# Optimization experiments

Hardware: AMD Instinct MI355X
Metric: run time of the kernel (lower is better)

## Reference

```python
import jax, jax.numpy as jnp
import numpy as np

N_NODES = 50000
N_EDGES = 1600000
N_GRAPHS = 512
NEG_SLOPE = 0.2


def _glorot(key, shape):
    fan_in, fan_out = shape[0], shape[-1]
    lim = jnp.sqrt(6.0 / (fan_in + fan_out))
    return jax.random.uniform(key, shape, jnp.float32, -lim, lim)


def setup_inputs() -> dict:
    key = jax.random.key(0)
    ks = jax.random.split(key, 12)
    x = jax.random.normal(ks[0], (N_NODES, 5), jnp.float32)
    edge_index = jax.random.randint(ks[1], (2, N_EDGES), 0, N_NODES, jnp.int64)
    batch = jnp.sort(jax.random.randint(ks[2], (N_NODES,), 0, N_GRAPHS, jnp.int64))
    # layer0: in=5 -> heads=4, out=16 (concat -> 64)
    W1l = _glorot(ks[3], (5, 64))
    W1r = _glorot(ks[4], (5, 64))
    att1 = _glorot(ks[5], (4, 16))
    b1 = jnp.zeros((64,), jnp.float32)
    # layer1: in=64 -> heads=1, out=64 (no concat)
    W2l = _glorot(ks[6], (64, 64))
    W2r = _glorot(ks[7], (64, 64))
    att2 = _glorot(ks[8], (1, 64))
    b2 = jnp.zeros((64,), jnp.float32)
    # predictor Linear(64, 1)
    Wp = _glorot(ks[9], (64, 1))
    bp = jnp.zeros((1,), jnp.float32)
    return {"x": x, "edge_index": edge_index, "batch": batch,
            "W1l": W1l, "W1r": W1r, "att1": att1, "b1": b1,
            "W2l": W2l, "W2r": W2r, "att2": att2, "b2": b2,
            "Wp": Wp, "bp": bp}


def _gatv2(x, src, dst, Wl, Wr, att, b, heads, dim, concat):
    n = x.shape[0]
    xl = (x @ Wl).reshape(n, heads, dim)  # source transform
    xr = (x @ Wr).reshape(n, heads, dim)  # target transform
    s = jax.nn.leaky_relu(xl[src] + xr[dst], NEG_SLOPE)      # [E,H,D]
    e = jnp.einsum('ehd,hd->eh', s, att)                      # [E,H]
    m = jax.ops.segment_max(e, dst, num_segments=n)           # segment softmax
    p = jnp.exp(e - m[dst])
    denom = jax.ops.segment_sum(p, dst, num_segments=n) + 1e-16
    alpha = p / denom[dst]                                    # [E,H]
    out = jax.ops.segment_sum(xl[src] * alpha[..., None], dst, num_segments=n)
    out = out.reshape(n, heads * dim) if concat else out.mean(axis=1)
    return out + b


def reference(x, edge_index, batch, W1l, W1r, att1, b1, W2l, W2r, att2, b2, Wp, bp):
    n = x.shape[0]
    # PyG GATv2Conv default add_self_loops=True
    loop = jnp.arange(n, dtype=edge_index.dtype)
    src = jnp.concatenate([edge_index[0], loop])
    dst = jnp.concatenate([edge_index[1], loop])
    h = _gatv2(x, src, dst, W1l, W1r, att1, b1, heads=4, dim=16, concat=True)
    h = jax.nn.relu(h)  # dropout is identity at eval
    h = _gatv2(h, src, dst, W2l, W2r, att2, b2, heads=1, dim=64, concat=False)
    h = jax.nn.relu(h)
    # global_mean_pool over graph ids
    sums = jax.ops.segment_sum(h, batch, num_segments=N_GRAPHS)
    cnt = jax.ops.segment_sum(jnp.ones((n,), h.dtype), batch, num_segments=N_GRAPHS)
    pooled = sums / jnp.maximum(cnt, 1.0)[:, None]
    return (pooled @ Wp + bp).squeeze(-1)
```

## Files before the change

kernel.cpp:

```cpp
#include <hip/hip_runtime.h>
#include <hip/hip_fp16.h>
#include <math.h>

#define NEG_SLOPE 0.2f
#define BUCKET 96

__device__ __forceinline__ float lrelu(float x) { return fmaxf(x, NEG_SLOPE * x); }

template <int CTRL>
__device__ __forceinline__ float dpp_add(float x) {
    int t = __builtin_amdgcn_update_dpp(0, __float_as_int(x), CTRL, 0xF, 0xF, false);
    return x + __int_as_float(t);
}

__device__ __forceinline__ float red8(float x) {
    x = dpp_add<0xB1>(x);
    x = dpp_add<0x4E>(x);
    x = dpp_add<0x141>(x);
    return x;
}

__device__ __forceinline__ float red32(float x) {
    x = red8(x);
    x = dpp_add<0x140>(x);
    x += __shfl_xor(x, 16, 64);
    return x;
}

__global__ void k_scatter(const int* __restrict__ ei, int* __restrict__ cnt,
                          int* __restrict__ ssrc, int E, int ET, int n, int nsub) {
    int part = blockIdx.x & 7;
    int sub  = blockIdx.x >> 3;
    int lo = (int)(((long long)part * n) >> 3);
    int hi = (int)(((long long)(part + 1) * n) >> 3);
    int stride = nsub * blockDim.x;
    for (int e = sub * blockDim.x + threadIdx.x; e < ET; e += stride) {
        int dst = (e < E) ? ei[E + e] : (e - E);
        if (dst >= lo && dst < hi) {
            int src = (e < E) ? ei[e] : dst;
            int pos = atomicAdd(&cnt[dst], 1);
            if (pos < BUCKET) ssrc[dst * BUCKET + pos] = src;
        }
    }
}

__global__ void k_t1(const float* __restrict__ x,
                     const float* __restrict__ W1l, const float* __restrict__ W1r,
                     __half* __restrict__ xl, float* __restrict__ xr, int n) {
    __shared__ float sWl[5 * 64], sWr[5 * 64];
    int t = threadIdx.x;
    for (int i = t; i < 5 * 64; i += blockDim.x) { sWl[i] = W1l[i]; sWr[i] = W1r[i]; }
    __syncthreads();
    int tid = blockIdx.x * blockDim.x + t;
    if (tid >= n * 64) return;
    int node = tid >> 6, j = tid & 63;
    const float* xp = x + node * 5;
    float x0 = xp[0], x1 = xp[1], x2 = xp[2], x3 = xp[3], x4 = xp[4];
    float al = x0 * sWl[j] + x1 * sWl[64 + j] + x2 * sWl[128 + j] + x3 * sWl[192 + j] + x4 * sWl[256 + j];
    float ar = x0 * sWr[j] + x1 * sWr[64 + j] + x2 * sWr[128 + j] + x3 * sWr[192 + j] + x4 * sWr[256 + j];
    xl[tid] = __float2half(al);
    xr[tid] = ar;
}

__global__ void __launch_bounds__(256, 8)
k_gat1(const int* __restrict__ ssrc, const int* __restrict__ deg,
       const __half* __restrict__ xl, const float* __restrict__ xr,
       const float* __restrict__ att1, const float* __restrict__ b1,
       const float* __restrict__ W2l, const float* __restrict__ W2r,
       __half* __restrict__ hl, float* __restrict__ hr, int n) {
    __shared__ float sh[4][64];
    int t = threadIdx.x;
    int wid = t >> 6, lane = t & 63;
    int node = __builtin_amdgcn_readfirstlane(blockIdx.x * 4 + wid);
    int half = lane >> 5, l31 = lane & 31;
    if (node < n) {
        float2 xrd  = *(const float2*)(xr + (size_t)node * 64 + 2 * l31);
        float2 attv = *(const float2*)(att1 + 2 * l31);
        float m = -INFINITY, den = 0.f, acc0 = 0.f, acc1 = 0.f;
        const int* bp_ = ssrc + (size_t)node * BUCKET;
        int end = deg[node]; if (end > BUCKET) end = BUCKET;
        int k = 0;
        for (; k + 15 < end; k += 16) {
            float2 a[8];
#pragma unroll
            for (int j = 0; j < 8; ++j) {
                int s0 = bp_[k + 2 * j], s1 = bp_[k + 2 * j + 1];
                int sj = half ? s1 : s0;
                a[j] = __half22float2(*(const __half2*)(xl + ((unsigned)sj << 6) + 2u * l31));
            }
            float s[8];
#pragma unroll
            for (int j = 0; j < 8; ++j)
                s[j] = lrelu(a[j].x + xrd.x) * attv.x + lrelu(a[j].y + xrd.y) * attv.y;
#pragma unroll
            for (int j = 0; j < 8; ++j) s[j] = red8(s[j]);
            float mb = fmaxf(fmaxf(fmaxf(s[0], s[1]), fmaxf(s[2], s[3])),
                             fmaxf(fmaxf(s[4], s[5]), fmaxf(s[6], s[7])));
            float mn = fmaxf(m, mb);
            float sc = __expf(m - mn);
            den *= sc; acc0 *= sc; acc1 *= sc;
#pragma unroll
            for (int j = 0; j < 8; ++j) {
                float p = __expf(s[j] - mn);
                den += p; acc0 += p * a[j].x; acc1 += p * a[j].y;
            }
            m = mn;
        }
        for (; k + 7 < end; k += 8) {
            float2 a[4];
#pragma unroll
            for (int j = 0; j < 4; ++j) {
                int s0 = bp_[k + 2 * j], s1 = bp_[k + 2 * j + 1];
                int sj = half ? s1 : s0;
                a[j] = __half22float2(*(const __half2*)(xl + ((unsigned)sj << 6) + 2u * l31));
            }
            float s[4];
#pragma unroll
            for (int j = 0; j < 4; ++j)
                s[j] = lrelu(a[j].x + xrd.x) * attv.x + lrelu(a[j].y + xrd.y) * attv.y;
#pragma unroll
            for (int j = 0; j < 4; ++j) s[j] = red8(s[j]);
            float mb = fmaxf(fmaxf(s[0], s[1]), fmaxf(s[2], s[3]));
            float mn = fmaxf(m, mb);
            float sc = __expf(m - mn);
            den *= sc; acc0 *= sc; acc1 *= sc;
#pragma unroll
            for (int j = 0; j < 4; ++j) {
                float p = __expf(s[j] - mn);
                den += p; acc0 += p * a[j].x; acc1 += p * a[j].y;
            }
            m = mn;
        }
        for (; k + 1 < end; k += 2) {
            int s0 = bp_[k], s1 = bp_[k + 1];
            int sj = half ? s1 : s0;
            float2 a = __half22float2(*(const __half2*)(xl + ((unsigned)sj << 6) + 2u * l31));
            float s = lrelu(a.x + xrd.x) * attv.x + lrelu(a.y + xrd.y) * attv.y;
            s = red8(s);
            float mn = fmaxf(m, s);
            float sc = __expf(m - mn);
            float p  = __expf(s - mn);
            den = den * sc + p;
            acc0 = acc0 * sc + p * a.x;
            acc1 = acc1 * sc + p * a.y;
            m = mn;
        }
        if (k < end) {
            int sj = bp_[k];
            float2 a = __half22float2(*(const __half2*)(xl + ((unsigned)sj << 6) + 2u * l31));
            float s = lrelu(a.x + xrd.x) * attv.x + lrelu(a.y + xrd.y) * attv.y;
            s = red8(s);
            if (half == 0) {
                float mn = fmaxf(m, s);
                float sc = __expf(m - mn);
                float p  = __expf(s - mn);
                den = den * sc + p;
                acc0 = acc0 * sc + p * a.x;
                acc1 = acc1 * sc + p * a.y;
                m = mn;
            }
        }
        float m_o  = __shfl_xor(m, 32, 64);
        float d_o  = __shfl_xor(den, 32, 64);
        float a0_o = __shfl_xor(acc0, 32, 64);
        float a1_o = __shfl_xor(acc1, 32, 64);
        float mf = fmaxf(m, m_o);
        float sc = __expf(m - mf), sco = __expf(m_o - mf);
        float denf = den * sc + d_o * sco + 1e-16f;
        float2 b = *(const float2*)(b1 + 2 * l31);
        float o0 = fmaxf((acc0 * sc + a0_o * sco) / denf + b.x, 0.f);
        float o1 = fmaxf((acc1 * sc + a1_o * sco) / denf + b.y, 0.f);
        if (half == 0) *(float2*)&sh[wid][2 * l31] = make_float2(o0, o1);
    }
    __syncthreads();
    if (node >= n) return;
    float accl = 0.f, accr = 0.f;
#pragma unroll 8
    for (int q = 0; q < 64; ++q) {
        float hv = sh[wid][q];
        accl += hv * W2l[q * 64 + lane];
        accr += hv * W2r[q * 64 + lane];
    }
    hl[(size_t)node * 64 + lane] = __float2half(accl);
    hr[(size_t)node * 64 + lane] = accr;
}

__global__ void __launch_bounds__(256, 8)
k_gat2(const int* __restrict__ ssrc, const int* __restrict__ deg,
       const __half* __restrict__ hl, const float* __restrict__ hr,
       const float* __restrict__ att2, const float* __restrict__ b2,
       const int* __restrict__ batch,
       float* __restrict__ pooled, float* __restrict__ cnt, int n) {
    int node = __builtin_amdgcn_readfirstlane((blockIdx.x * blockDim.x + threadIdx.x) >> 6);
    if (node >= n) return;
    int lane = threadIdx.x & 63;
    int half = lane >> 5, l31 = lane & 31;
    float2 hrd  = *(const float2*)(hr + (size_t)node * 64 + 2 * l31);
    float2 attv = *(const float2*)(att2 + 2 * l31);
    float m = -INFINITY, den = 0.f, acc0 = 0.f, acc1 = 0.f;
    const int* bp_ = ssrc + (size_t)node * BUCKET;
    int end = deg[node]; if (end > BUCKET) end = BUCKET;
    int k = 0;
    for (; k + 15 < end; k += 16) {
        float2 a[8];
#pragma unroll
        for (int j = 0; j < 8; ++j) {
            int s0 = bp_[k + 2 * j], s1 = bp_[k + 2 * j + 1];
            int sj = half ? s1 : s0;
            a[j] = __half22float2(*(const __half2*)(hl + ((unsigned)sj << 6) + 2u * l31));
        }
        float s[8];
#pragma unroll
        for (int j = 0; j < 8; ++j)
            s[j] = lrelu(a[j].x + hrd.x) * attv.x + lrelu(a[j].y + hrd.y) * attv.y;
#pragma unroll
        for (int j = 0; j < 8; ++j) s[j] = red32(s[j]);
        float mb = fmaxf(fmaxf(fmaxf(s[0], s[1]), fmaxf(s[2], s[3])),
                         fmaxf(fmaxf(s[4], s[5]), fmaxf(s[6], s[7])));
        float mn = fmaxf(m, mb);
        float sc = __expf(m - mn);
        den *= sc; acc0 *= sc; acc1 *= sc;
#pragma unroll
        for (int j = 0; j < 8; ++j) {
            float p = __expf(s[j] - mn);
            den += p; acc0 += p * a[j].x; acc1 += p * a[j].y;
        }
        m = mn;
    }
    for (; k + 7 < end; k += 8) {
        float2 a[4];
#pragma unroll
        for (int j = 0; j < 4; ++j) {
            int s0 = bp_[k + 2 * j], s1 = bp_[k + 2 * j + 1];
            int sj = half ? s1 : s0;
            a[j] = __half22float2(*(const __half2*)(hl + ((unsigned)sj << 6) + 2u * l31));
        }
        float s[4];
#pragma unroll
        for (int j = 0; j < 4; ++j)
            s[j] = lrelu(a[j].x + hrd.x) * attv.x + lrelu(a[j].y + hrd.y) * attv.y;
#pragma unroll
        for (int j = 0; j < 4; ++j) s[j] = red32(s[j]);
        float mb = fmaxf(fmaxf(s[0], s[1]), fmaxf(s[2], s[3]));
        float mn = fmaxf(m, mb);
        float sc = __expf(m - mn);
        den *= sc; acc0 *= sc; acc1 *= sc;
#pragma unroll
        for (int j = 0; j < 4; ++j) {
            float p = __expf(s[j] - mn);
            den += p; acc0 += p * a[j].x; acc1 += p * a[j].y;
        }
        m = mn;
    }
    for (; k + 1 < end; k += 2) {
        int s0 = bp_[k], s1 = bp_[k + 1];
        int sj = half ? s1 : s0;
        float2 a = __half22float2(*(const __half2*)(hl + ((unsigned)sj << 6) + 2u * l31));
        float s = lrelu(a.x + hrd.x) * attv.x + lrelu(a.y + hrd.y) * attv.y;
        s = red32(s);
        float mn = fmaxf(m, s);
        float sc = __expf(m - mn);
        float p  = __expf(s - mn);
        den = den * sc + p;
        acc0 = acc0 * sc + p * a.x;
        acc1 = acc1 * sc + p * a.y;
        m = mn;
    }
    if (k < end) {
        int sj = bp_[k];
        float2 a = __half22float2(*(const __half2*)(hl + ((unsigned)sj << 6) + 2u * l31));
        float s = lrelu(a.x + hrd.x) * attv.x + lrelu(a.y + hrd.y) * attv.y;
        s = red32(s);
        if (half == 0) {
            float mn = fmaxf(m, s);
            float sc = __expf(m - mn);
            float p  = __expf(s - mn);
            den = den * sc + p;
            acc0 = acc0 * sc + p * a.x;
            acc1 = acc1 * sc + p * a.y;
            m = mn;
        }
    }
    float m_o  = __shfl_xor(m, 32, 64);
    float d_o  = __shfl_xor(den, 32, 64);
    float a0_o = __shfl_xor(acc0, 32, 64);
    float a1_o = __shfl_xor(acc1, 32, 64);
    float mf = fmaxf(m, m_o);
    float sc = __expf(m - mf), sco = __expf(m_o - mf);
    float denf = den * sc + d_o * sco + 1e-16f;
    float2 b = *(const float2*)(b2 + 2 * l31);
    float o0 = fmaxf((acc0 * sc + a0_o * sco) / denf + b.x, 0.f);
    float o1 = fmaxf((acc1 * sc + a1_o * sco) / denf + b.y, 0.f);
    int g = batch[node];
    atomicAdd(&pooled[(size_t)g * 64 + 2 * l31 + half], half ? o1 : o0);
    if (lane == 0) atomicAdd(&cnt[g], 1.0f);
}

__global__ void k_predict(const float* __restrict__ pooled, const float* __restrict__ cnt,
                          const float* __restrict__ Wp, const float* __restrict__ bp,
                          float* __restrict__ out, int G) {
    int tid = blockIdx.x * blockDim.x + threadIdx.x;
    int g = tid >> 6;
    if (g >= G) return;
    int lane = threadIdx.x & 63;
    float c = cnt[g];
    if (c < 1.f) c = 1.f;
    float v = (pooled[(size_t)g * 64 + lane] / c) * Wp[lane];
#pragma unroll
    for (int off = 32; off > 0; off >>= 1) v += __shfl_down(v, off, 64);
    if (lane == 0) out[g] = v + bp[0];
}

extern "C" void kernel_launch(void* const* d_in, const int* in_sizes, int n_in,
                              void* d_out, int out_size, void* d_ws, size_t ws_size,
                              hipStream_t stream) {
    const float* x    = (const float*)d_in[0];
    const int*   ei   = (const int*)d_in[1];
    const int*   batch= (const int*)d_in[2];
    const float* W1l  = (const float*)d_in[3];
    const float* W1r  = (const float*)d_in[4];
    const float* att1 = (const float*)d_in[5];
    const float* b1   = (const float*)d_in[6];
    const float* W2l  = (const float*)d_in[7];
    const float* W2r  = (const float*)d_in[8];
    const float* att2 = (const float*)d_in[9];
    const float* b2   = (const float*)d_in[10];
    const float* Wp   = (const float*)d_in[11];
    const float* bp   = (const float*)d_in[12];
    float* out = (float*)d_out;

    const int n  = in_sizes[0] / 5;
    const int E  = in_sizes[1] / 2;
    const int ET = E + n;
    const int G  = out_size;

    char* ws = (char*)d_ws;
    size_t off = 0;
    auto alloc_b = [&](size_t bytes) { void* p = (void*)(ws + off); off += (bytes + 15) & ~15ull; return p; };
    __half* xl    = (__half*)alloc_b((size_t)n * 64 * 2);
    float*  xr    = (float*)alloc_b((size_t)n * 64 * 4);
    __half* hl    = (__half*)alloc_b((size_t)n * 64 * 2);
    float*  hr    = (float*)alloc_b((size_t)n * 64 * 4);
    float*  pooled= (float*)alloc_b((size_t)G * 64 * 4);
    float*  cntf  = (float*)alloc_b((size_t)G * 4);
    int*    deg   = (int*)alloc_b((size_t)n * 4);
    int*    ssrc  = (int*)alloc_b((size_t)n * BUCKET * 4);

    size_t zero_bytes = (size_t)((char*)deg - (char*)pooled) + (size_t)n * 4;
    (void)hipMemsetAsync(pooled, 0, zero_bytes, stream);

    const int B = 256;
    const int NSUB = 256;

    k_scatter<<<8 * NSUB, B, 0, stream>>>(ei, deg, ssrc, E, ET, n, NSUB);

    k_t1<<<(n * 64 + B - 1) / B, B, 0, stream>>>(x, W1l, W1r, xl, xr, n);

    k_gat1<<<(n + 3) / 4, B, 0, stream>>>(ssrc, deg, xl, xr, att1, b1, W2l, W2r, hl, hr, n);
    k_gat2<<<((size_t)n * 64 + B - 1) / B, B, 0, stream>>>(ssrc, deg, hl, hr, att2, b2, batch, pooled, cntf, n);
    k_predict<<<(G * 64 + B - 1) / B, B, 0, stream>>>(pooled, cntf, Wp, bp, out, G);
}
```

Baseline: 358.4 us.

## Process 8 edges per wave with 8 lanes each using 16-byte gathers

After: 382.7 us. 1.07x slower.

```diff
diff --git a/kernel.cpp b/kernel.cpp
--- a/kernel.cpp
+++ b/kernel.cpp
@@ -17,13 +17,6 @@
     x = dpp_add<0xB1>(x);
     x = dpp_add<0x4E>(x);
     x = dpp_add<0x141>(x);
-    return x;
-}
-
-__device__ __forceinline__ float red32(float x) {
-    x = red8(x);
-    x = dpp_add<0x140>(x);
-    x += __shfl_xor(x, 16, 64);
     return x;
 }
 
@@ -62,7 +55,7 @@
     xr[tid] = ar;
 }
 
-__global__ void __launch_bounds__(256, 8)
+__global__ void __launch_bounds__(256, 5)
 k_gat1(const int* __restrict__ ssrc, const int* __restrict__ deg,
        const __half* __restrict__ xl, const float* __restrict__ xr,
        const float* __restrict__ att1, const float* __restrict__ b1,
@@ -72,105 +65,100 @@
     int t = threadIdx.x;
     int wid = t >> 6, lane = t & 63;
     int node = __builtin_amdgcn_readfirstlane(blockIdx.x * 4 + wid);
-    int half = lane >> 5, l31 = lane & 31;
+    int g = lane >> 3, c = lane & 7;
     if (node < n) {
-        float2 xrd  = *(const float2*)(xr + (size_t)node * 64 + 2 * l31);
-        float2 attv = *(const float2*)(att1 + 2 * l31);
-        float m = -INFINITY, den = 0.f, acc0 = 0.f, acc1 = 0.f;
+        float xrd[8], attv[8];
+        {
+            float4 v0 = *(const float4*)(xr + (size_t)node * 64 + 8 * c);
+            float4 v1 = *(const float4*)(xr + (size_t)node * 64 + 8 * c + 4);
+            xrd[0] = v0.x; xrd[1] = v0.y; xrd[2] = v0.z; xrd[3] = v0.w;
+            xrd[4] = v1.x; xrd[5] = v1.y; xrd[6] = v1.z; xrd[7] = v1.w;
+            float4 a0 = *(const float4*)(att1 + 8 * c);
+            float4 a1 = *(const float4*)(att1 + 8 * c + 4);
+            attv[0] = a0.x; attv[1] = a0.y; attv[2] = a0.z; attv[3] = a0.w;
+            attv[4] = a1.x; attv[5] = a1.y; attv[6] = a1.z; attv[7] = a1.w;
+        }
+        float m = -1e30f, den = 0.f;
+        float acc[8];
+#pragma unroll
+        for (int d = 0; d < 8; ++d) acc[d] = 0.f;
         const int* bp_ = ssrc + (size_t)node * BUCKET;
         int end = deg[node]; if (end > BUCKET) end = BUCKET;
-        int k = 0;
-        for (; k + 15 < end; k += 16) {
-            float2 a[8];
-#pragma unroll
-            for (int j = 0; j < 8; ++j) {
-                int s0 = bp_[k + 2 * j], s1 = bp_[k + 2 * j + 1];
-                int sj = half ? s1 : s0;
-                a[j] = __half22float2(*(const __half2*)(xl + ((unsigned)sj << 6) + 2u * l31));
+        int idx[4];
+#pragma unroll
+        for (int j = 0; j < 4; ++j) { int e = 8 * j + g; idx[j] = bp_[e < end ? e : 0]; }
+        for (int k = 0; k < end; k += 32) {
+            float4 raw[4];
+#pragma unroll
+            for (int j = 0; j < 4; ++j)
+                raw[j] = *(const float4*)((const char*)xl + (((size_t)(unsigned)idx[j]) << 7) + ((unsigned)c << 4));
+            int kn = k + 32;
+            if (kn < end) {
+#pragma unroll
+                for (int j = 0; j < 4; ++j) { int e = kn + 8 * j + g; idx[j] = bp_[e < end ? e : 0]; }
             }
-            float s[8];
-#pragma unroll
-            for (int j = 0; j < 8; ++j)
-                s[j] = lrelu(a[j].x + xrd.x) * attv.x + lrelu(a[j].y + xrd.y) * attv.y;
-#pragma unroll
-            for (int j = 0; j < 8; ++j) s[j] = red8(s[j]);
-            float mb = fmaxf(fmaxf(fmaxf(s[0], s[1]), fmaxf(s[2], s[3])),
-                             fmaxf(fmaxf(s[4], s[5]), fmaxf(s[6], s[7])));
+            float av[4][8], s[4];
+            bool vl[4];
+#pragma unroll
+            for (int j = 0; j < 4; ++j) {
+                vl[j] = (k + 8 * j + g) < end;
+                const __half2* hp = (const __half2*)&raw[j];
+#pragma unroll
+                for (int q = 0; q < 4; ++q) {
+                    float2 f = __half22float2(hp[q]);
+                    av[j][2 * q] = f.x; av[j][2 * q + 1] = f.y;
+                }
+                float sj = 0.f;
+#pragma unroll
+                for (int d = 0; d < 8; ++d) sj += lrelu(av[j][d] + xrd[d]) * attv[d];
+                s[j] = dpp_add<0xB1>(sj);
+            }
+            float mb = fmaxf(fmaxf(vl[0] ? s[0] : -1e30f, vl[1] ? s[1] : -1e30f),
+                             fmaxf(vl[2] ? s[2] : -1e30f, vl[3] ? s[3] : -1e30f));
             float mn = fmaxf(m, mb);
             float sc = __expf(m - mn);
-            den *= sc; acc0 *= sc; acc1 *= sc;
-#pragma unroll
-            for (int j = 0; j < 8; ++j) {
-                float p = __expf(s[j] - mn);
-                den += p; acc0 += p * a[j].x; acc1 += p * a[j].y;
+            den *= sc;
+#pragma unroll
+            for (int d = 0; d < 8; ++d) acc[d] *= sc;
+#pragma unroll
+            for (int j = 0; j < 4; ++j) {
+                float p = vl[j] ? __expf(s[j] - mn) : 0.f;
+                den += p;
+#pragma unroll
+                for (int d = 0; d < 8; ++d) acc[d] += p * av[j][d];
             }
             m = mn;
         }
-        for (; k + 7 < end; k += 8) {
-            float2 a[4];
-#pragma unroll
-            for (int j = 0; j < 4; ++j) {
-                int s0 = bp_[k + 2 * j], s1 = bp_[k + 2 * j + 1];
-                int sj = half ? s1 : s0;
-                a[j] = __half22float2(*(const __half2*)(xl + ((unsigned)sj << 6) + 2u * l31));
-            }
-            float s[4];
-#pragma unroll
-            for (int j = 0; j < 4; ++j)
-                s[j] = lrelu(a[j].x + xrd.x) * attv.x + lrelu(a[j].y + xrd.y) * attv.y;
-#pragma unroll
-            for (int j = 0; j < 4; ++j) s[j] = red8(s[j]);
-            float mb = fmaxf(fmaxf(s[0], s[1]), fmaxf(s[2], s[3]));
-            float mn = fmaxf(m, mb);
-            float sc = __expf(m - mn);
-            den *= sc; acc0 *= sc; acc1 *= sc;
-#pragma unroll
-            for (int j = 0; j < 4; ++j) {
-                float p = __expf(s[j] - mn);
-                den += p; acc0 += p * a[j].x; acc1 += p * a[j].y;
-            }
-            m = mn;
-        }
-        for (; k + 1 < end; k += 2) {
-            int s0 = bp_[k], s1 = bp_[k + 1];
-            int sj = half ? s1 : s0;
-            float2 a = __half22float2(*(const __half2*)(xl + ((unsigned)sj << 6) + 2u * l31));
-            float s = lrelu(a.x + xrd.x) * attv.x + lrelu(a.y + xrd.y) * attv.y;
-            s = red8(s);
-            float mn = fmaxf(m, s);
-            float sc = __expf(m - mn);
-            float p  = __expf(s - mn);
-            den = den * sc + p;
-            acc0 = acc0 * sc + p * a.x;
-            acc1 = acc1 * sc + p * a.y;
-            m = mn;
-        }
-        if (k < end) {
-            int sj = bp_[k];
-            float2 a = __half22float2(*(const __half2*)(xl + ((unsigned)sj << 6) + 2u * l31));
-            float s = lrelu(a.x + xrd.x) * attv.x + lrelu(a.y + xrd.y) * attv.y;
-            s = red8(s);
-            if (half == 0) {
-                float mn = fmaxf(m, s);
-                float sc = __expf(m - mn);
-                float p  = __expf(s - mn);
-                den = den * sc + p;
-                acc0 = acc0 * sc + p * a.x;
-                acc1 = acc1 * sc + p * a.y;
-                m = mn;
-            }
-        }
-        float m_o  = __shfl_xor(m, 32, 64);
-        float d_o  = __shfl_xor(den, 32, 64);
-        float a0_o = __shfl_xor(acc0, 32, 64);
-        float a1_o = __shfl_xor(acc1, 32, 64);
-        float mf = fmaxf(m, m_o);
-        float sc = __expf(m - mf), sco = __expf(m_o - mf);
-        float denf = den * sc + d_o * sco + 1e-16f;
-        float2 b = *(const float2*)(b1 + 2 * l31);
-        float o0 = fmaxf((acc0 * sc + a0_o * sco) / denf + b.x, 0.f);
-        float o1 = fmaxf((acc1 * sc + a1_o * sco) / denf + b.y, 0.f);
-        if (half == 0) *(float2*)&sh[wid][2 * l31] = make_float2(o0, o1);
+#pragma unroll
+        for (int off = 8; off <= 32; off <<= 1) {
+            float m_o = __shfl_xor(m, off, 64);
+            float d_o = __shfl_xor(den, off, 64);
+            float a_o[8];
+#pragma unroll
+            for (int d = 0; d < 8; ++d) a_o[d] = __shfl_xor(acc[d], off, 64);
+            float mf = fmaxf(m, m_o);
+            float s0 = __expf(m - mf), s1 = __expf(m_o - mf);
+            den = den * s0 + d_o * s1;
+#pragma unroll
+            for (int d = 0; d < 8; ++d) acc[d] = acc[d] * s0 + a_o[d] * s1;
+            m = mf;
+        }
+        float denf = den + 1e-16f;
+        if (g == 0) {
+            float4 b0 = *(const float4*)(b1 + 8 * c);
+            float4 b1v = *(const float4*)(b1 + 8 * c + 4);
+            float4 o0, o1;
+            o0.x = fmaxf(acc[0] / denf + b0.x, 0.f);
+            o0.y = fmaxf(acc[1] / denf + b0.y, 0.f);
+            o0.z = fmaxf(acc[2] / denf + b0.z, 0.f);
+            o0.w = fmaxf(acc[3] / denf + b0.w, 0.f);
+            o1.x = fmaxf(acc[4] / denf + b1v.x, 0.f);
+            o1.y = fmaxf(acc[5] / denf + b1v.y, 0.f);
+            o1.z = fmaxf(acc[6] / denf + b1v.z, 0.f);
+            o1.w = fmaxf(acc[7] / denf + b1v.w, 0.f);
+            *(float4*)&sh[wid][8 * c]     = o0;
+            *(float4*)&sh[wid][8 * c + 4] = o1;
+        }
     }
     __syncthreads();
     if (node >= n) return;
@@ -185,7 +173,7 @@
     hr[(size_t)node * 64 + lane] = accr;
 }
 
-__global__ void __launch_bounds__(256, 8)
+__global__ void __launch_bounds__(256, 5)
 k_gat2(const int* __restrict__ ssrc, const int* __restrict__ deg,
        const __half* __restrict__ hl, const float* __restrict__ hr,
        const float* __restrict__ att2, const float* __restrict__ b2,
@@ -194,106 +182,92 @@
     int node = __builtin_amdgcn_readfirstlane((blockIdx.x * blockDim.x + threadIdx.x) >> 6);
     if (node >= n) return;
     int lane = threadIdx.x & 63;
-    int half = lane >> 5, l31 = lane & 31;
-    float2 hrd  = *(const float2*)(hr + (size_t)node * 64 + 2 * l31);
-    float2 attv = *(const float2*)(att2 + 2 * l31);
-    float m = -INFINITY, den = 0.f, acc0 = 0.f, acc1 = 0.f;
+    int g = lane >> 3, c = lane & 7;
+    float hrd[8], attv[8];
+    {
+        float4 v0 = *(const float4*)(hr + (size_t)node * 64 + 8 * c);
+        float4 v1 = *(const float4*)(hr + (size_t)node * 64 + 8 * c + 4);
+        hrd[0] = v0.x; hrd[1] = v0.y; hrd[2] = v0.z; hrd[3] = v0.w;
+        hrd[4] = v1.x; hrd[5] = v1.y; hrd[6] = v1.z; hrd[7] = v1.w;
+        float4 a0 = *(const float4*)(att2 + 8 * c);
+        float4 a1 = *(const float4*)(att2 + 8 * c + 4);
+        attv[0] = a0.x; attv[1] = a0.y; attv[2] = a0.z; attv[3] = a0.w;
+        attv[4] = a1.x; attv[5] = a1.y; attv[6] = a1.z; attv[7] = a1.w;
+    }
+    float m = -1e30f, den = 0.f;
+    float acc[8];
+#pragma unroll
+    for (int d = 0; d < 8; ++d) acc[d] = 0.f;
     const int* bp_ = ssrc + (size_t)node * BUCKET;
     int end = deg[node]; if (end > BUCKET) end = BUCKET;
-    int k = 0;
-    for (; k + 15 < end; k += 16) {
-        float2 a[8];
-#pragma unroll
-        for (int j = 0; j < 8; ++j) {
-            int s0 = bp_[k + 2 * j], s1 = bp_[k + 2 * j + 1];
-            int sj = half ? s1 : s0;
-            a[j] = __half22float2(*(const __half2*)(hl + ((unsigned)sj << 6) + 2u * l31));
-        }
-        float s[8];
-#pragma unroll
-        for (int j = 0; j < 8; ++j)
-            s[j] = lrelu(a[j].x + hrd.x) * attv.x + lrelu(a[j].y + hrd.y) * attv.y;
-#pragma unroll
-        for (int j = 0; j < 8; ++j) s[j] = red32(s[j]);
-        float mb = fmaxf(fmaxf(fmaxf(s[0], s[1]), fmaxf(s[2], s[3])),
-                         fmaxf(fmaxf(s[4], s[5]), fmaxf(s[6], s[7])));
+    int idx[4];
+#pragma unroll
+    for (int j = 0; j < 4; ++j) { int e = 8 * j + g; idx[j] = bp_[e < end ? e : 0]; }
+    for (int k = 0; k < end; k += 32) {
+        float4 raw[4];
+#pragma unroll
+        for (int j = 0; j < 4; ++j)
+            raw[j] = *(const float4*)((const char*)hl + (((size_t)(unsigned)idx[j]) << 7) + ((unsigned)c << 4));
+        int kn = k + 32;
+        if (kn < end) {
+#pragma unroll
+            for (int j = 0; j < 4; ++j) { int e = kn + 8 * j + g; idx[j] = bp_[e < end ? e : 0]; }
+        }
+        float av[4][8], s[4];
+        bool vl[4];
+#pragma unroll
+        for (int j = 0; j < 4; ++j) {
+            vl[j] = (k + 8 * j + g) < end;
+            const __half2* hp = (const __half2*)&raw[j];
+#pragma unroll
+            for (int q = 0; q < 4; ++q) {
+                float2 f = __half22float2(hp[q]);
+                av[j][2 * q] = f.x; av[j][2 * q + 1] = f.y;
+            }
+            float sj = 0.f;
+#pragma unroll
+            for (int d = 0; d < 8; ++d) sj += lrelu(av[j][d] + hrd[d]) * attv[d];
+            s[j] = red8(sj);
+        }
+        float mb = fmaxf(fmaxf(vl[0] ? s[0] : -1e30f, vl[1] ? s[1] : -1e30f),
+                         fmaxf(vl[2] ? s[2] : -1e30f, vl[3] ? s[3] : -1e30f));
         float mn = fmaxf(m, mb);
         float sc = __expf(m - mn);
-        den *= sc; acc0 *= sc; acc1 *= sc;
-#pragma unroll
-        for (int j = 0; j < 8; ++j) {
-            float p = __expf(s[j] - mn);
-            den += p; acc0 += p * a[j].x; acc1 += p * a[j].y;
+        den *= sc;
+#pragma unroll
+        for (int d = 0; d < 8; ++d) acc[d] *= sc;
+#pragma unroll
+        for (int j = 0; j < 4; ++j) {
+            float p = vl[j] ? __expf(s[j] - mn) : 0.f;
+            den += p;
+#pragma unroll
+            for (int d = 0; d < 8; ++d) acc[d] += p * av[j][d];
         }
         m = mn;
     }
-    for (; k + 7 < end; k += 8) {
-        float2 a[4];
-#pragma unroll
-        for (int j = 0; j < 4; ++j) {
-            int s0 = bp_[k + 2 * j], s1 = bp_[k + 2 * j + 1];
-            int sj = half ? s1 : s0;
-            a[j] = __half22float2(*(const __half2*)(hl + ((unsigned)sj << 6) + 2u * l31));
-        }
-        float s[4];
-#pragma unroll
-        for (int j = 0; j < 4; ++j)
-            s[j] = lrelu(a[j].x + hrd.x) * attv.x + lrelu(a[j].y + hrd.y) * attv.y;
-#pragma unroll
-        for (int j = 0; j < 4; ++j) s[j] = red32(s[j]);
-        float mb = fmaxf(fmaxf(s[0], s[1]), fmaxf(s[2], s[3]));
-        float mn = fmaxf(m, mb);
-        float sc = __expf(m - mn);
-        den *= sc; acc0 *= sc; acc1 *= sc;
-#pragma unroll
-        for (int j = 0; j < 4; ++j) {
-            float p = __expf(s[j] - mn);
-            den += p; acc0 += p * a[j].x; acc1 += p * a[j].y;
-        }
-        m = mn;
-    }
-    for (; k + 1 < end; k += 2) {
-        int s0 = bp_[k], s1 = bp_[k + 1];
-        int sj = half ? s1 : s0;
-        float2 a = __half22float2(*(const __half2*)(hl + ((unsigned)sj << 6) + 2u * l31));
-        float s = lrelu(a.x + hrd.x) * attv.x + lrelu(a.y + hrd.y) * attv.y;
-        s = red32(s);
-        float mn = fmaxf(m, s);
-        float sc = __expf(m - mn);
-        float p  = __expf(s - mn);
-        den = den * sc + p;
-        acc0 = acc0 * sc + p * a.x;
-        acc1 = acc1 * sc + p * a.y;
-        m = mn;
-    }
-    if (k < end) {
-        int sj = bp_[k];
-        float2 a = __half22float2(*(const __half2*)(hl + ((unsigned)sj << 6) + 2u * l31));
-        float s = lrelu(a.x + hrd.x) * attv.x + lrelu(a.y + hrd.y) * attv.y;
-        s = red32(s);
-        if (half == 0) {
-            float mn = fmaxf(m, s);
-            float sc = __expf(m - mn);
-            float p  = __expf(s - mn);
-            den = den * sc + p;
-            acc0 = acc0 * sc + p * a.x;
-            acc1 = acc1 * sc + p * a.y;
-            m = mn;
-        }
-    }
-    float m_o  = __shfl_xor(m, 32, 64);
-    float d_o  = __shfl_xor(den, 32, 64);
-    float a0_o = __shfl_xor(acc0, 32, 64);
-    float a1_o = __shfl_xor(acc1, 32, 64);
-    float mf = fmaxf(m, m_o);
-    float sc = __expf(m - mf), sco = __expf(m_o - mf);
-    float denf = den * sc + d_o * sco + 1e-16f;
-    float2 b = *(const float2*)(b2 + 2 * l31);
-    float o0 = fmaxf((acc0 * sc + a0_o * sco) / denf + b.x, 0.f);
-    float o1 = fmaxf((acc1 * sc + a1_o * sco) / denf + b.y, 0.f);
-    int g = batch[node];
-    atomicAdd(&pooled[(size_t)g * 64 + 2 * l31 + half], half ? o1 : o0);
-    if (lane == 0) atomicAdd(&cnt[g], 1.0f);
+#pragma unroll
+    for (int off = 8; off <= 32; off <<= 1) {
+        float m_o = __shfl_xor(m, off, 64);
+        float d_o = __shfl_xor(den, off, 64);
+        float a_o[8];
+#pragma unroll
+        for (int d = 0; d < 8; ++d) a_o[d] = __shfl_xor(acc[d], off, 64);
+        float mf = fmaxf(m, m_o);
+        float s0 = __expf(m - mf), s1 = __expf(m_o - mf);
+        den = den * s0 + d_o * s1;
+#pragma unroll
+        for (int d = 0; d < 8; ++d) acc[d] = acc[d] * s0 + a_o[d] * s1;
+        m = mf;
+    }
+    float denf = den + 1e-16f;
+    float v = acc[0];
+#pragma unroll
+    for (int q = 1; q < 8; ++q) v = (g == q) ? acc[q] : v;
+    float bsel = b2[8 * c + g];
+    v = fmaxf(v / denf + bsel, 0.f);
+    int gr = batch[node];
+    atomicAdd(&pooled[(size_t)gr * 64 + 8 * c + g], v);
+    if (lane == 0) atomicAdd(&cnt[gr], 1.0f);
 }
 
 __global__ void k_predict(const float* __restrict__ pooled, const float* __restrict__ cnt,
```

## Process two destination nodes per wave in GAT layer-2 aggregation

Applied to the files above, without the earlier changes.

Result: faster. 345.5 us (-3.6%).

```diff
diff --git a/kernel.cpp b/kernel.cpp
--- a/kernel.cpp
+++ b/kernel.cpp
@@ -185,47 +185,47 @@
     hr[(size_t)node * 64 + lane] = accr;
 }
 
-__global__ void __launch_bounds__(256, 8)
-k_gat2(const int* __restrict__ ssrc, const int* __restrict__ deg,
-       const __half* __restrict__ hl, const float* __restrict__ hr,
-       const float* __restrict__ att2, const float* __restrict__ b2,
-       const int* __restrict__ batch,
-       float* __restrict__ pooled, float* __restrict__ cnt, int n) {
-    int node = __builtin_amdgcn_readfirstlane((blockIdx.x * blockDim.x + threadIdx.x) >> 6);
-    if (node >= n) return;
-    int lane = threadIdx.x & 63;
-    int half = lane >> 5, l31 = lane & 31;
-    float2 hrd  = *(const float2*)(hr + (size_t)node * 64 + 2 * l31);
-    float2 attv = *(const float2*)(att2 + 2 * l31);
-    float m = -INFINITY, den = 0.f, acc0 = 0.f, acc1 = 0.f;
-    const int* bp_ = ssrc + (size_t)node * BUCKET;
-    int end = deg[node]; if (end > BUCKET) end = BUCKET;
-    int k = 0;
+
+__device__ __forceinline__ void load16(const int* __restrict__ bp_, int k,
+                                       const __half* __restrict__ hl,
+                                       int half, int l31, float2* a) {
+#pragma unroll
+    for (int j = 0; j < 8; ++j) {
+        int s0 = bp_[k + 2 * j], s1 = bp_[k + 2 * j + 1];
+        int sj = half ? s1 : s0;
+        a[j] = __half22float2(*(const __half2*)(hl + ((unsigned)sj << 6) + 2u * l31));
+    }
+}
+
+__device__ __forceinline__ void upd16(const float2* a, float2 hrd, float2 attv,
+                                      float& m, float& den, float& acc0, float& acc1) {
+    float s[8];
+#pragma unroll
+    for (int j = 0; j < 8; ++j)
+        s[j] = lrelu(a[j].x + hrd.x) * attv.x + lrelu(a[j].y + hrd.y) * attv.y;
+#pragma unroll
+    for (int j = 0; j < 8; ++j) s[j] = red32(s[j]);
+    float mb = fmaxf(fmaxf(fmaxf(s[0], s[1]), fmaxf(s[2], s[3])),
+                     fmaxf(fmaxf(s[4], s[5]), fmaxf(s[6], s[7])));
+    float mn = fmaxf(m, mb);
+    float sc = __expf(m - mn);
+    den *= sc; acc0 *= sc; acc1 *= sc;
+#pragma unroll
+    for (int j = 0; j < 8; ++j) {
+        float p = __expf(s[j] - mn);
+        den += p; acc0 += p * a[j].x; acc1 += p * a[j].y;
+    }
+    m = mn;
+}
+
+__device__ __forceinline__ void gat2_tail(const int* __restrict__ bp_, int k, int end,
+                                          const __half* __restrict__ hl,
+                                          float2 hrd, float2 attv, int half, int l31,
+                                          float& m, float& den, float& acc0, float& acc1) {
     for (; k + 15 < end; k += 16) {
         float2 a[8];
-#pragma unroll
-        for (int j = 0; j < 8; ++j) {
-            int s0 = bp_[k + 2 * j], s1 = bp_[k + 2 * j + 1];
-            int sj = half ? s1 : s0;
-            a[j] = __half22float2(*(const __half2*)(hl + ((unsigned)sj << 6) + 2u * l31));
-        }
-        float s[8];
-#pragma unroll
-        for (int j = 0; j < 8; ++j)
-            s[j] = lrelu(a[j].x + hrd.x) * attv.x + lrelu(a[j].y + hrd.y) * attv.y;
-#pragma unroll
-        for (int j = 0; j < 8; ++j) s[j] = red32(s[j]);
-        float mb = fmaxf(fmaxf(fmaxf(s[0], s[1]), fmaxf(s[2], s[3])),
-                         fmaxf(fmaxf(s[4], s[5]), fmaxf(s[6], s[7])));
-        float mn = fmaxf(m, mb);
-        float sc = __expf(m - mn);
-        den *= sc; acc0 *= sc; acc1 *= sc;
-#pragma unroll
-        for (int j = 0; j < 8; ++j) {
-            float p = __expf(s[j] - mn);
-            den += p; acc0 += p * a[j].x; acc1 += p * a[j].y;
-        }
-        m = mn;
+        load16(bp_, k, hl, half, l31, a);
+        upd16(a, hrd, attv, m, den, acc0, acc1);
     }
     for (; k + 7 < end; k += 8) {
         float2 a[4];
@@ -281,6 +281,13 @@
             m = mn;
         }
     }
+}
+
+__device__ __forceinline__ void gat2_finish(float m, float den, float acc0, float acc1,
+                                            const float* __restrict__ b2,
+                                            const int* __restrict__ batch, int node,
+                                            float* __restrict__ pooled, float* __restrict__ cnt,
+                                            int lane, int half, int l31) {
     float m_o  = __shfl_xor(m, 32, 64);
     float d_o  = __shfl_xor(den, 32, 64);
     float a0_o = __shfl_xor(acc0, 32, 64);
@@ -291,9 +298,46 @@
     float2 b = *(const float2*)(b2 + 2 * l31);
     float o0 = fmaxf((acc0 * sc + a0_o * sco) / denf + b.x, 0.f);
     float o1 = fmaxf((acc1 * sc + a1_o * sco) / denf + b.y, 0.f);
-    int g = batch[node];
-    atomicAdd(&pooled[(size_t)g * 64 + 2 * l31 + half], half ? o1 : o0);
-    if (lane == 0) atomicAdd(&cnt[g], 1.0f);
+    int gr = batch[node];
+    atomicAdd(&pooled[(size_t)gr * 64 + 2 * l31 + half], half ? o1 : o0);
+    if (lane == 0) atomicAdd(&cnt[gr], 1.0f);
+}
+
+__global__ void __launch_bounds__(256, 6)
+k_gat2(const int* __restrict__ ssrc, const int* __restrict__ deg,
+       const __half* __restrict__ hl, const float* __restrict__ hr,
+       const float* __restrict__ att2, const float* __restrict__ b2,
+       const int* __restrict__ batch,
+       float* __restrict__ pooled, float* __restrict__ cnt, int n) {
+    int wave = __builtin_amdgcn_readfirstlane((blockIdx.x * blockDim.x + threadIdx.x) >> 6);
+    int nA = wave * 2;
+    if (nA >= n) return;
+    int nB = nA + 1;
+    bool hasB = (nB < n);
+    int lane = threadIdx.x & 63;
+    int half = lane >> 5, l31 = lane & 31;
+    float2 attv = *(const float2*)(att2 + 2 * l31);
+    float2 hrdA = *(const float2*)(hr + (size_t)nA * 64 + 2 * l31);
+    float2 hrdB = hasB ? *(const float2*)(hr + (size_t)nB * 64 + 2 * l31) : make_float2(0.f, 0.f);
+    const int* bpA = ssrc + (size_t)nA * BUCKET;
+    const int* bpB = ssrc + (size_t)nB * BUCKET;
+    int endA = deg[nA]; if (endA > BUCKET) endA = BUCKET;
+    int endB = hasB ? deg[nB] : 0; if (endB > BUCKET) endB = BUCKET;
+    float mA = -INFINITY, denA = 0.f, a0A = 0.f, a1A = 0.f;
+    float mB = -INFINITY, denB = 0.f, a0B = 0.f, a1B = 0.f;
+    int endmin = endA < endB ? endA : endB;
+    int k = 0;
+    for (; k + 15 < endmin; k += 16) {
+        float2 aA[8], aB[8];
+        load16(bpA, k, hl, half, l31, aA);
+        load16(bpB, k, hl, half, l31, aB);
+        upd16(aA, hrdA, attv, mA, denA, a0A, a1A);
+        upd16(aB, hrdB, attv, mB, denB, a0B, a1B);
+    }
+    gat2_tail(bpA, k, endA, hl, hrdA, attv, half, l31, mA, denA, a0A, a1A);
+    if (hasB) gat2_tail(bpB, k, endB, hl, hrdB, attv, half, l31, mB, denB, a0B, a1B);
+    gat2_finish(mA, denA, a0A, a1A, b2, batch, nA, pooled, cnt, lane, half, l31);
+    if (hasB) gat2_finish(mB, denB, a0B, a1B, b2, batch, nB, pooled, cnt, lane, half, l31);
 }
 
 __global__ void k_predict(const float* __restrict__ pooled, const float* __restrict__ cnt,
@@ -357,6 +401,9 @@
     k_t1<<<(n * 64 + B - 1) / B, B, 0, stream>>>(x, W1l, W1r, xl, xr, n);
 
     k_gat1<<<(n + 3) / 4, B, 0, stream>>>(ssrc, deg, xl, xr, att1, b1, W2l, W2r, hl, hr, n);
-    k_gat2<<<((size_t)n * 64 + B - 1) / B, B, 0, stream>>>(ssrc, deg, hl, hr, att2, b2, batch, pooled, cntf, n);
+    {
+        int nwaves = (n + 1) / 2;
+        k_gat2<<<(nwaves + 3) / 4, B, 0, stream>>>(ssrc, deg, hl, hr, att2, b2, batch, pooled, cntf, n);
+    }
     k_predict<<<(G * 64 + B - 1) / B, B, 0, stream>>>(pooled, cntf, Wp, bp, out, G);
 }
```

## Gather raw 5-dim features in layer 1 and store source indices as 16-bit

Applied to the files above, without the earlier changes.

After: 405.4 us. 1.13x slower.

```diff
diff --git a/kernel.cpp b/kernel.cpp
--- a/kernel.cpp
+++ b/kernel.cpp
@@ -4,6 +4,7 @@
 
 #define NEG_SLOPE 0.2f
 #define BUCKET 96
+typedef unsigned short ushort_t;
 
 __device__ __forceinline__ float lrelu(float x) { return fmaxf(x, NEG_SLOPE * x); }
 
@@ -28,7 +29,7 @@
 }
 
 __global__ void k_scatter(const int* __restrict__ ei, int* __restrict__ cnt,
-                          int* __restrict__ ssrc, int E, int ET, int n, int nsub) {
+                          ushort_t* __restrict__ ssrc, int E, int ET, int n, int nsub) {
     int part = blockIdx.x & 7;
     int sub  = blockIdx.x >> 3;
     int lo = (int)(((long long)part * n) >> 3);
@@ -39,32 +40,31 @@
         if (dst >= lo && dst < hi) {
             int src = (e < E) ? ei[e] : dst;
             int pos = atomicAdd(&cnt[dst], 1);
-            if (pos < BUCKET) ssrc[dst * BUCKET + pos] = src;
-        }
-    }
-}
-
-__global__ void k_t1(const float* __restrict__ x,
-                     const float* __restrict__ W1l, const float* __restrict__ W1r,
-                     __half* __restrict__ xl, float* __restrict__ xr, int n) {
-    __shared__ float sWl[5 * 64], sWr[5 * 64];
+            if (pos < BUCKET) ssrc[dst * BUCKET + pos] = (ushort_t)src;
+        }
+    }
+}
+
+__global__ void k_t1(const float* __restrict__ x, const float* __restrict__ W1r,
+                     __half* __restrict__ xp16, float* __restrict__ xr, int n) {
+    __shared__ float sWr[5 * 64];
     int t = threadIdx.x;
-    for (int i = t; i < 5 * 64; i += blockDim.x) { sWl[i] = W1l[i]; sWr[i] = W1r[i]; }
+    for (int i = t; i < 5 * 64; i += blockDim.x) sWr[i] = W1r[i];
     __syncthreads();
     int tid = blockIdx.x * blockDim.x + t;
     if (tid >= n * 64) return;
     int node = tid >> 6, j = tid & 63;
     const float* xp = x + node * 5;
     float x0 = xp[0], x1 = xp[1], x2 = xp[2], x3 = xp[3], x4 = xp[4];
-    float al = x0 * sWl[j] + x1 * sWl[64 + j] + x2 * sWl[128 + j] + x3 * sWl[192 + j] + x4 * sWl[256 + j];
     float ar = x0 * sWr[j] + x1 * sWr[64 + j] + x2 * sWr[128 + j] + x3 * sWr[192 + j] + x4 * sWr[256 + j];
-    xl[tid] = __float2half(al);
     xr[tid] = ar;
+    if (j < 8) xp16[node * 8 + j] = (j < 5) ? __float2half(xp[j]) : __float2half(0.f);
 }
 
 __global__ void __launch_bounds__(256, 8)
-k_gat1(const int* __restrict__ ssrc, const int* __restrict__ deg,
-       const __half* __restrict__ xl, const float* __restrict__ xr,
+k_gat1(const ushort_t* __restrict__ ssrc, const int* __restrict__ deg,
+       const __half* __restrict__ xp16, const float* __restrict__ xr,
+       const float* __restrict__ W1l,
        const float* __restrict__ att1, const float* __restrict__ b1,
        const float* __restrict__ W2l, const float* __restrict__ W2r,
        __half* __restrict__ hl, float* __restrict__ hr, int n) {
@@ -76,48 +76,34 @@
     if (node < n) {
         float2 xrd  = *(const float2*)(xr + (size_t)node * 64 + 2 * l31);
         float2 attv = *(const float2*)(att1 + 2 * l31);
+        float2 w0 = *(const float2*)(W1l +   0 + 2 * l31);
+        float2 w1 = *(const float2*)(W1l +  64 + 2 * l31);
+        float2 w2 = *(const float2*)(W1l + 128 + 2 * l31);
+        float2 w3 = *(const float2*)(W1l + 192 + 2 * l31);
+        float2 w4 = *(const float2*)(W1l + 256 + 2 * l31);
         float m = -INFINITY, den = 0.f, acc0 = 0.f, acc1 = 0.f;
-        const int* bp_ = ssrc + (size_t)node * BUCKET;
+        const ushort_t* bp_ = ssrc + (size_t)node * BUCKET;
         int end = deg[node]; if (end > BUCKET) end = BUCKET;
         int k = 0;
-        for (; k + 15 < end; k += 16) {
-            float2 a[8];
-#pragma unroll
-            for (int j = 0; j < 8; ++j) {
-                int s0 = bp_[k + 2 * j], s1 = bp_[k + 2 * j + 1];
-                int sj = half ? s1 : s0;
-                a[j] = __half22float2(*(const __half2*)(xl + ((unsigned)sj << 6) + 2u * l31));
-            }
-            float s[8];
-#pragma unroll
-            for (int j = 0; j < 8; ++j)
-                s[j] = lrelu(a[j].x + xrd.x) * attv.x + lrelu(a[j].y + xrd.y) * attv.y;
-#pragma unroll
-            for (int j = 0; j < 8; ++j) s[j] = red8(s[j]);
-            float mb = fmaxf(fmaxf(fmaxf(s[0], s[1]), fmaxf(s[2], s[3])),
-                             fmaxf(fmaxf(s[4], s[5]), fmaxf(s[6], s[7])));
-            float mn = fmaxf(m, mb);
-            float sc = __expf(m - mn);
-            den *= sc; acc0 *= sc; acc1 *= sc;
-#pragma unroll
-            for (int j = 0; j < 8; ++j) {
-                float p = __expf(s[j] - mn);
-                den += p; acc0 += p * a[j].x; acc1 += p * a[j].y;
-            }
-            m = mn;
-        }
         for (; k + 7 < end; k += 8) {
-            float2 a[4];
+            uint4 xx[4];
 #pragma unroll
             for (int j = 0; j < 4; ++j) {
                 int s0 = bp_[k + 2 * j], s1 = bp_[k + 2 * j + 1];
                 int sj = half ? s1 : s0;
-                a[j] = __half22float2(*(const __half2*)(xl + ((unsigned)sj << 6) + 2u * l31));
+                xx[j] = *(const uint4*)(xp16 + ((unsigned)sj << 3));
             }
-            float s[4];
-#pragma unroll
-            for (int j = 0; j < 4; ++j)
-                s[j] = lrelu(a[j].x + xrd.x) * attv.x + lrelu(a[j].y + xrd.y) * attv.y;
+            float2 a[4]; float s[4];
+#pragma unroll
+            for (int j = 0; j < 4; ++j) {
+                float2 f01 = __half22float2(*(const __half2*)&xx[j].x);
+                float2 f23 = __half22float2(*(const __half2*)&xx[j].y);
+                float2 f4  = __half22float2(*(const __half2*)&xx[j].z);
+                float ax = f01.x * w0.x + f01.y * w1.x + f23.x * w2.x + f23.y * w3.x + f4.x * w4.x;
+                float ay = f01.x * w0.y + f01.y * w1.y + f23.x * w2.y + f23.y * w3.y + f4.x * w4.y;
+                a[j] = make_float2(ax, ay);
+                s[j] = lrelu(ax + xrd.x) * attv.x + lrelu(ay + xrd.y) * attv.y;
+            }
 #pragma unroll
             for (int j = 0; j < 4; ++j) s[j] = red8(s[j]);
             float mb = fmaxf(fmaxf(s[0], s[1]), fmaxf(s[2], s[3]));
@@ -134,29 +120,39 @@
         for (; k + 1 < end; k += 2) {
             int s0 = bp_[k], s1 = bp_[k + 1];
             int sj = half ? s1 : s0;
-            float2 a = __half22float2(*(const __half2*)(xl + ((unsigned)sj << 6) + 2u * l31));
-            float s = lrelu(a.x + xrd.x) * attv.x + lrelu(a.y + xrd.y) * attv.y;
+            uint4 xx = *(const uint4*)(xp16 + ((unsigned)sj << 3));
+            float2 f01 = __half22float2(*(const __half2*)&xx.x);
+            float2 f23 = __half22float2(*(const __half2*)&xx.y);
+            float2 f4  = __half22float2(*(const __half2*)&xx.z);
+            float ax = f01.x * w0.x + f01.y * w1.x + f23.x * w2.x + f23.y * w3.x + f4.x * w4.x;
+            float ay = f01.x * w0.y + f01.y * w1.y + f23.x * w2.y + f23.y * w3.y + f4.x * w4.y;
+            float s = lrelu(ax + xrd.x) * attv.x + lrelu(ay + xrd.y) * attv.y;
             s = red8(s);
             float mn = fmaxf(m, s);
             float sc = __expf(m - mn);
             float p  = __expf(s - mn);
             den = den * sc + p;
-            acc0 = acc0 * sc + p * a.x;
-            acc1 = acc1 * sc + p * a.y;
+            acc0 = acc0 * sc + p * ax;
+            acc1 = acc1 * sc + p * ay;
             m = mn;
         }
         if (k < end) {
             int sj = bp_[k];
-            float2 a = __half22float2(*(const __half2*)(xl + ((unsigned)sj << 6) + 2u * l31));
-            float s = lrelu(a.x + xrd.x) * attv.x + lrelu(a.y + xrd.y) * attv.y;
+            uint4 xx = *(const uint4*)(xp16 + ((unsigned)sj << 3));
+            float2 f01 = __half22float2(*(const __half2*)&xx.x);
+            float2 f23 = __half22float2(*(const __half2*)&xx.y);
+            float2 f4  = __half22float2(*(const __half2*)&xx.z);
+            float ax = f01.x * w0.x + f01.y * w1.x + f23.x * w2.x + f23.y * w3.x + f4.x * w4.x;
+            float ay = f01.x * w0.y + f01.y * w1.y + f23.x * w2.y + f23.y * w3.y + f4.x * w4.y;
+            float s = lrelu(ax + xrd.x) * attv.x + lrelu(ay + xrd.y) * attv.y;
             s = red8(s);
             if (half == 0) {
                 float mn = fmaxf(m, s);
                 float sc = __expf(m - mn);
                 float p  = __expf(s - mn);
                 den = den * sc + p;
-                acc0 = acc0 * sc + p * a.x;
-                acc1 = acc1 * sc + p * a.y;
+                acc0 = acc0 * sc + p * ax;
+                acc1 = acc1 * sc + p * ay;
                 m = mn;
             }
         }
@@ -186,7 +182,7 @@
 }
 
 __global__ void __launch_bounds__(256, 8)
-k_gat2(const int* __restrict__ ssrc, const int* __restrict__ deg,
+k_gat2(const ushort_t* __restrict__ ssrc, const int* __restrict__ deg,
        const __half* __restrict__ hl, const float* __restrict__ hr,
        const float* __restrict__ att2, const float* __restrict__ b2,
        const int* __restrict__ batch,
@@ -198,7 +194,7 @@
     float2 hrd  = *(const float2*)(hr + (size_t)node * 64 + 2 * l31);
     float2 attv = *(const float2*)(att2 + 2 * l31);
     float m = -INFINITY, den = 0.f, acc0 = 0.f, acc1 = 0.f;
-    const int* bp_ = ssrc + (size_t)node * BUCKET;
+    const ushort_t* bp_ = ssrc + (size_t)node * BUCKET;
     int end = deg[node]; if (end > BUCKET) end = BUCKET;
     int k = 0;
     for (; k + 15 < end; k += 16) {
@@ -337,14 +333,14 @@
     char* ws = (char*)d_ws;
     size_t off = 0;
     auto alloc_b = [&](size_t bytes) { void* p = (void*)(ws + off); off += (bytes + 15) & ~15ull; return p; };
-    __half* xl    = (__half*)alloc_b((size_t)n * 64 * 2);
+    __half* xp16  = (__half*)alloc_b((size_t)n * 8 * 2);
     float*  xr    = (float*)alloc_b((size_t)n * 64 * 4);
     __half* hl    = (__half*)alloc_b((size_t)n * 64 * 2);
     float*  hr    = (float*)alloc_b((size_t)n * 64 * 4);
     float*  pooled= (float*)alloc_b((size_t)G * 64 * 4);
     float*  cntf  = (float*)alloc_b((size_t)G * 4);
     int*    deg   = (int*)alloc_b((size_t)n * 4);
-    int*    ssrc  = (int*)alloc_b((size_t)n * BUCKET * 4);
+    ushort_t* ssrc= (ushort_t*)alloc_b((size_t)n * BUCKET * 2);
 
     size_t zero_bytes = (size_t)((char*)deg - (char*)pooled) + (size_t)n * 4;
     (void)hipMemsetAsync(pooled, 0, zero_bytes, stream);
@@ -354,9 +350,9 @@
 
     k_scatter<<<8 * NSUB, B, 0, stream>>>(ei, deg, ssrc, E, ET, n, NSUB);
 
-    k_t1<<<(n * 64 + B - 1) / B, B, 0, stream>>>(x, W1l, W1r, xl, xr, n);
-
-    k_gat1<<<(n + 3) / 4, B, 0, stream>>>(ssrc, deg, xl, xr, att1, b1, W2l, W2r, hl, hr, n);
+    k_t1<<<(n * 64 + B - 1) / B, B, 0, stream>>>(x, W1r, xp16, xr, n);
+
+    k_gat1<<<(n + 3) / 4, B, 0, stream>>>(ssrc, deg, xp16, xr, W1l, att1, b1, W2l, W2r, hl, hr, n);
     k_gat2<<<((size_t)n * 64 + B - 1) / B, B, 0, stream>>>(ssrc, deg, hl, hr, att2, b2, batch, pooled, cntf, n);
     k_predict<<<(G * 64 + B - 1) / B, B, 0, stream>>>(pooled, cntf, Wp, bp, out, G);
 }
```
